# Kernel optimization log

Hardware: AMD Instinct MI355X
Metric: run time of the kernel (lower is better)

## Reference

```python
import jax, jax.numpy as jnp
from jax import lax
import numpy as np

T, N, E = 8, 20000, 640000
D_IN, H, K = 2, 64, 3


def setup_inputs() -> dict:
    key = jax.random.key(0)
    ks = jax.random.split(key, 10)
    x = jax.random.normal(ks[0], (T, N, D_IN), dtype=jnp.float32)
    edge_idx = jax.random.randint(ks[1], (T, 2, E), 0, N, dtype=jnp.int64)
    edge_attr = jax.random.uniform(ks[2], (T, E), dtype=jnp.float32)
    Fin = D_IN + H
    s = 0.05
    Wr = jax.random.normal(ks[3], (K, Fin, H), dtype=jnp.float32) * s
    Wu = jax.random.normal(ks[4], (K, Fin, H), dtype=jnp.float32) * s
    Wc = jax.random.normal(ks[5], (K, Fin, H), dtype=jnp.float32) * s
    br = jnp.zeros((H,), dtype=jnp.float32)
    bu = jnp.zeros((H,), dtype=jnp.float32)
    bc = jnp.zeros((H,), dtype=jnp.float32)
    return {"x": x, "edge_idx": edge_idx, "edge_attr": edge_attr,
            "Wr": Wr, "br": br, "Wu": Wu, "bu": bu, "Wc": Wc, "bc": bc}


def reference(x, edge_idx, edge_attr, Wr, br, Wu, bu, Wc, bc):
    n = x.shape[1]
    k_hops = Wr.shape[0]

    def cheb(v, src, dst, wn, W, b):
        # Chebyshev recursion on scaled Laplacian (PyG ChebConv, lambda_max=2)
        def prop(t):
            return jax.ops.segment_sum(wn[:, None] * t[src], dst, num_segments=n)
        Tx0 = v
        out = Tx0 @ W[0]
        Tx1 = prop(Tx0)
        out = out + Tx1 @ W[1]
        for kk in range(2, k_hops):
            Tx2 = 2.0 * prop(Tx1) - Tx0
            out = out + Tx2 @ W[kk]
            Tx0, Tx1 = Tx1, Tx2
        return out + b

    def step(h, inp):
        x_t, ei, w_t = inp
        src, dst = ei[0], ei[1]
        # sym-normalized Laplacian, scaled by 2/lambda_max=1; self-loop weight is 0
        deg = jax.ops.segment_sum(w_t, src, num_segments=n)
        safe = jnp.where(deg > 0, deg, 1.0)
        dinv = jnp.where(deg > 0, lax.rsqrt(safe), 0.0)
        wn = -dinv[src] * w_t * dinv[dst]
        comb = jnp.concatenate([x_t, h], axis=1)
        r = jax.nn.sigmoid(cheb(comb, src, dst, wn, Wr, br))
        u = jax.nn.sigmoid(cheb(comb, src, dst, wn, Wu, bu))
        c = jnp.tanh(cheb(jnp.concatenate([x_t, r * h], axis=1), src, dst, wn, Wc, bc))
        h_new = u * h + (1.0 - u) * c
        return h_new, None

    h0 = jnp.zeros((n, br.shape[0]), dtype=x.dtype)
    h_final, _ = lax.scan(step, h0, (x, edge_idx, edge_attr))
    return h_final
```

## Files before the change

### kernel.cpp

```cpp
#include <hip/hip_runtime.h>

#define NN 20000
#define EE 640000
#define TT 8
#define HF 64
#define AS 232
#define ACS 104
#define BSS 194
#define PBLK 5000
#define TILE 2560
#define NBIN 250
#define BWID 80
#define ECAP 3072
#define LCAP 24

typedef _Float16 f16;
typedef unsigned int uint;
typedef unsigned char uchar;
typedef __attribute__((ext_vector_type(8))) _Float16 half8;
typedef __attribute__((ext_vector_type(4))) float floatx4;

__device__ __forceinline__ float lo16f(uint v) { return (float)__builtin_bit_cast(f16, (unsigned short)(v & 0xffff)); }
__device__ __forceinline__ float hi16f(uint v) { return (float)__builtin_bit_cast(f16, (unsigned short)(v >> 16)); }
__device__ __forceinline__ uint pk16(float a, float b) {
    unsigned short ua = __builtin_bit_cast(unsigned short, (f16)a);
    unsigned short ub = __builtin_bit_cast(unsigned short, (f16)b);
    return (uint)ua | ((uint)ub << 16);
}

__global__ __launch_bounds__(256) void k_prepW(
    const float* __restrict__ Wr, const float* __restrict__ Wu, const float* __restrict__ Wc,
    f16* __restrict__ Wp, f16* __restrict__ Wcp)
{
    int idx = blockIdx.x * 256 + threadIdx.x;
    if (idx < 8 * 7 * 64) {
        int lane = idx & 63;
        int kb = (idx >> 6) % 7;
        int nb = (idx >> 6) / 7;
        int col = nb * 16 + (lane & 15);
        int g = col >> 6, jj = col & 63;
        const float* W = (g == 0) ? Wr : Wu;
        half8 v;
        #pragma unroll
        for (int e = 0; e < 8; e++) {
            int k = kb * 32 + ((lane >> 4) << 3) + e;
            float val = 0.f;
            if (k < 192)      { int hop = k >> 6; int i = 2 + (k & 63); val = W[(hop * 66 + i) * 64 + jj]; }
            else if (k < 198) { int q = k - 192;  int hop = q >> 1;     val = W[(hop * 66 + (q & 1)) * 64 + jj]; }
            v[e] = (f16)val;
        }
        *(half8*)&Wp[(size_t)idx * 8] = v;
        return;
    }
    int idx2 = idx - 8 * 7 * 64;
    if (idx2 >= 12 * 3 * 64) return;
    int lane = idx2 & 63;
    int kb = (idx2 >> 6) % 3;
    int nbc = (idx2 >> 6) / 3;
    int col = nbc * 16 + (lane & 15);
    int mode = col >> 6, j = col & 63;
    half8 v;
    #pragma unroll
    for (int e = 0; e < 8; e++) {
        int k = kb * 32 + ((lane >> 4) << 3) + e;
        float val = 0.f;
        if (k < 66) {
            if (mode == 0)      val = Wc[(0 * 66 + k) * 64 + j] - Wc[(2 * 66 + k) * 64 + j];
            else if (mode == 1) val = Wc[(1 * 66 + k) * 64 + j];
            else                val = Wc[(2 * 66 + k) * 64 + j];
        }
        v[e] = (f16)val;
    }
    *(half8*)&Wcp[(size_t)idx2 * 8] = v;
}

__global__ __launch_bounds__(256) void k_pack(
    const float* __restrict__ x, uint* __restrict__ xf)
{
    int idx = blockIdx.x * 256 + threadIdx.x;
    if (idx < TT * NN) xf[idx] = pk16(x[2 * idx], x[2 * idx + 1]);
}

__global__ __launch_bounds__(256) void k_bin(
    const int* __restrict__ eidx, const float* __restrict__ eatt,
    int* __restrict__ binptr, uint2* __restrict__ ebuf,
    int* __restrict__ sbinptr, uint* __restrict__ sbuf)
{
    __shared__ uint2 buf[NBIN][LCAP];
    __shared__ uint  sbl[NBIN][LCAP];
    __shared__ int lcnt[NBIN], scnt[NBIN];
    __shared__ int scan[256];
    __shared__ int gb[NBIN];
    int tid = threadIdx.x;
    if (tid < NBIN) { lcnt[tid] = 0; scnt[tid] = 0; }
    __syncthreads();
    int tl = blockIdx.x / 250, tile = blockIdx.x % 250;
    const int*   src = eidx + (size_t)tl * 2 * EE + tile * TILE;
    const int*   dst = src + EE;
    const float* w   = eatt + (size_t)tl * EE + tile * TILE;
    int* bp = binptr + tl * NBIN;
    int* sp = sbinptr + tl * NBIN;
    size_t ebase = (size_t)tl * NBIN * ECAP;
    #pragma unroll
    for (int i = 0; i < TILE / 256; i++) {
        int e = i * 256 + tid;
        int s = __builtin_nontemporal_load(&src[e]);
        int d = __builtin_nontemporal_load(&dst[e]);
        float wv = __builtin_nontemporal_load(&w[e]);
        int bin = d / BWID;
        uint2 ent = make_uint2(((uint)d << 16) | (uint)s, __float_as_uint(wv));
        int p = atomicAdd(&lcnt[bin], 1);
        if (p < LCAP) buf[bin][p] = ent;
        else {
            int gp = atomicAdd(&bp[bin], 1);
            if (gp < ECAP) ebuf[ebase + (size_t)bin * ECAP + gp] = ent;
        }
        int sbin = s / BWID;
        uint sent = (pk16(wv, 0.f) << 16) | (uint)s;
        int sq = atomicAdd(&scnt[sbin], 1);
        if (sq < LCAP) sbl[sbin][sq] = sent;
        else {
            int gp = atomicAdd(&sp[sbin], 1);
            if (gp < ECAP) sbuf[ebase + (size_t)sbin * ECAP + gp] = sent;
        }
    }
    __syncthreads();
    {
        int c = (tid < NBIN) ? (lcnt[tid] < LCAP ? lcnt[tid] : LCAP) : 0;
        scan[tid] = c;
        __syncthreads();
        #pragma unroll
        for (int o = 1; o < 256; o <<= 1) {
            int v = (tid >= o) ? scan[tid - o] : 0;
            __syncthreads();
            scan[tid] += v;
            __syncthreads();
        }
        if (c > 0) gb[tid] = atomicAdd(&bp[tid], c);
        __syncthreads();
        int total = scan[255];
        for (int i = tid; i < total; i += 256) {
            int lo = 0, hi = 255;
            #pragma unroll
            for (int it = 0; it < 8; it++) { int mid = (lo + hi) >> 1; if (scan[mid] > i) hi = mid; else lo = mid + 1; }
            int p = i - (lo ? scan[lo - 1] : 0);
            int gp = gb[lo] + p;
            if (gp < ECAP) ebuf[ebase + (size_t)lo * ECAP + gp] = buf[lo][p];
        }
    }
    __syncthreads();
    {
        int c = (tid < NBIN) ? (scnt[tid] < LCAP ? scnt[tid] : LCAP) : 0;
        scan[tid] = c;
        __syncthreads();
        #pragma unroll
        for (int o = 1; o < 256; o <<= 1) {
            int v = (tid >= o) ? scan[tid - o] : 0;
            __syncthreads();
            scan[tid] += v;
            __syncthreads();
        }
        if (c > 0) gb[tid] = atomicAdd(&sp[tid], c);
        __syncthreads();
        int total = scan[255];
        for (int i = tid; i < total; i += 256) {
            int lo = 0, hi = 255;
            #pragma unroll
            for (int it = 0; it < 8; it++) { int mid = (lo + hi) >> 1; if (scan[mid] > i) hi = mid; else lo = mid + 1; }
            int p = i - (lo ? scan[lo - 1] : 0);
            int gp = gb[lo] + p;
            if (gp < ECAP) sbuf[ebase + (size_t)lo * ECAP + gp] = sbl[lo][p];
        }
    }
}

__global__ __launch_bounds__(256) void k_degred(
    const uint* __restrict__ sbuf, const int* __restrict__ sbinptr,
    float* __restrict__ dinv)
{
    __shared__ float dacc[BWID];
    int tl = blockIdx.x / NBIN, b = blockIdx.x % NBIN, tid = threadIdx.x;
    int nume = sbinptr[tl * NBIN + b]; if (nume > ECAP) nume = ECAP;
    if (tid < BWID) dacc[tid] = 0.f;
    __syncthreads();
    size_t base = (size_t)(tl * NBIN + b) * ECAP;
    for (int i = tid; i < nume; i += 256) {
        uint e = sbuf[base + i];
        atomicAdd(&dacc[(e & 0xffff) - b * BWID], hi16f(e));
    }
    __syncthreads();
    if (tid < BWID) {
        float d = dacc[tid];
        dinv[(size_t)tl * NN + b * BWID + tid] = d > 0.f ? 1.f / sqrtf(d) : 0.f;
    }
}

__global__ __launch_bounds__(256) void k_csr(
    const uint2* __restrict__ ebuf, const int* __restrict__ binptr,
    const float* __restrict__ dinv,
    uint* __restrict__ entries, int* __restrict__ row_ptr, int* __restrict__ cnt)
{
    __shared__ uint proc[ECAP];
    __shared__ uchar lnb[ECAP];
    __shared__ uint staged[ECAP];
    __shared__ int lcnt[BWID], loff[BWID];
    int tl = blockIdx.x / NBIN, b = blockIdx.x % NBIN, tid = threadIdx.x;
    int nume = binptr[tl * NBIN + b]; if (nume > ECAP) nume = ECAP;
    const float* dv = dinv + (size_t)tl * NN;
    size_t base = (size_t)(tl * NBIN + b) * ECAP;
    if (tid < BWID) lcnt[tid] = 0;
    __syncthreads();
    for (int i = tid; i < nume; i += 256) {
        uint2 ent = ebuf[base + i];
        int s = ent.x & 0xffff;
        int d = ent.x >> 16;
        float wv = __uint_as_float(ent.y);
        float wn = -dv[s] * wv * dv[d];
        unsigned short wb = __builtin_bit_cast(unsigned short, (f16)wn);
        proc[i] = ((uint)wb << 16) | (uint)s;
        int ln = d - b * BWID;
        lnb[i] = (uchar)ln;
        atomicAdd(&lcnt[ln], 1);
    }
    __syncthreads();
    if (tid == 0) {
        int run = 0;
        for (int i = 0; i < BWID; i++) { loff[i] = run; run += lcnt[i]; }
    }
    __syncthreads();
    if (tid < BWID) {
        int n = tl * NN + b * BWID + tid;
        row_ptr[n] = (int)base + loff[tid];
        cnt[n] = lcnt[tid];
    }
    __syncthreads();
    for (int i = tid; i < nume; i += 256) {
        int p = atomicAdd(&loff[lnb[i]], 1);
        staged[p] = proc[i];
    }
    __syncthreads();
    for (int i = tid; i < nume; i += 256)
        entries[base + i] = staged[i];
}

__device__ __forceinline__ void gather64(
    const f16* __restrict__ src_mat, const uint* wnb, int mp, int j, int q,
    float& s0, float& s1)
{
    float a0[8], a1[8];
    #pragma unroll
    for (int k = 0; k < 8; k++) { a0[k] = 0.f; a1[k] = 0.f; }
    int e = 0;
    for (; e + 16 <= mp; e += 16) {
        uint ee[8], rr[8];
        #pragma unroll
        for (int k = 0; k < 8; k++) ee[k] = wnb[e + 2 * k + q];
        #pragma unroll
        for (int k = 0; k < 8; k++) rr[k] = *(const uint*)&src_mat[(size_t)(ee[k] & 0xffff) * HF + 2 * j];
        #pragma unroll
        for (int k = 0; k < 8; k++) {
            float w = hi16f(ee[k]);
            a0[k] += w * lo16f(rr[k]);
            a1[k] += w * hi16f(rr[k]);
        }
    }
    for (; e < mp; e += 8) {
        uint ee[4], rr[4];
        #pragma unroll
        for (int k = 0; k < 4; k++) ee[k] = wnb[e + 2 * k + q];
        #pragma unroll
        for (int k = 0; k < 4; k++) rr[k] = *(const uint*)&src_mat[(size_t)(ee[k] & 0xffff) * HF + 2 * j];
        #pragma unroll
        for (int k = 0; k < 4; k++) {
            float w = hi16f(ee[k]);
            a0[k] += w * lo16f(rr[k]);
            a1[k] += w * hi16f(rr[k]);
        }
    }
    s0 = ((a0[0] + a0[1]) + (a0[2] + a0[3])) + ((a0[4] + a0[5]) + (a0[6] + a0[7]));
    s1 = ((a1[0] + a1[1]) + (a1[2] + a1[3])) + ((a1[4] + a1[5]) + (a1[6] + a1[7]));
    s0 += __shfl_xor(s0, 32);
    s1 += __shfl_xor(s1, 32);
}

__global__ __launch_bounds__(256) void k_prop(
    const f16* __restrict__ src_mat, const f16* __restrict__ base,
    f16* __restrict__ dst,
    const int* __restrict__ row_ptr, const int* __restrict__ cnt,
    const uint* __restrict__ entries,
    float alpha, float beta,
    const uint* __restrict__ xsrc, const uint* __restrict__ xbase,
    uint* __restrict__ xdst)
{
    __shared__ uint wnbuf[4][128];
    int ws = threadIdx.x >> 6, lane = threadIdx.x & 63;
    int node = blockIdx.x * 4 + ws;
    int m = cnt[node]; if (m > 128) m = 128;
    int st = row_ptr[node];
    int mp = (m + 7) & ~7;
    for (int idx = lane; idx < mp; idx += 64)
        wnbuf[ws][idx] = (idx < m) ? entries[st + idx] : 0u;
    asm volatile("s_waitcnt lgkmcnt(0)" ::: "memory");

    int j = lane & 31, q = lane >> 5;
    float s0, s1;
    gather64(src_mat, wnbuf[ws], mp, j, q, s0, s1);
    if (q == 0) {
        float r0 = alpha * s0, r1 = alpha * s1;
        if (base) {
            uint bv = *(const uint*)&base[(size_t)node * HF + 2 * j];
            r0 += beta * lo16f(bv);
            r1 += beta * hi16f(bv);
        }
        *(uint*)&dst[(size_t)node * HF + 2 * j] = pk16(r0, r1);
    }

    if (xdst) {
        float xa0 = 0.f, xa1 = 0.f;
        for (int i = lane; i < mp; i += 64) {
            uint ent = wnbuf[ws][i];
            uint xv = xsrc[ent & 0xffff];
            float wn = hi16f(ent);
            xa0 += wn * lo16f(xv);
            xa1 += wn * hi16f(xv);
        }
        #pragma unroll
        for (int o = 32; o >= 1; o >>= 1) {
            xa0 += __shfl_xor(xa0, o);
            xa1 += __shfl_xor(xa1, o);
        }
        if (lane == 0) {
            float r0 = alpha * xa0, r1 = alpha * xa1;
            if (xbase) { uint bv = xbase[node]; r0 += beta * lo16f(bv); r1 += beta * hi16f(bv); }
            xdst[node] = pk16(r0, r1);
        }
    }
}

__global__ __launch_bounds__(256) void k_prop_fin(
    const f16* __restrict__ S, const f16* __restrict__ B0,
    const f16* __restrict__ u, const float* __restrict__ h_in,
    float* __restrict__ h_out, f16* __restrict__ hA_out,
    const int* __restrict__ row_ptr, const int* __restrict__ cnt,
    const uint* __restrict__ entries)
{
    __shared__ uint wnbuf[4][128];
    int ws = threadIdx.x >> 6, lane = threadIdx.x & 63;
    int node = blockIdx.x * 4 + ws;
    int m = cnt[node]; if (m > 128) m = 128;
    int st = row_ptr[node];
    int mp = (m + 7) & ~7;
    for (int idx = lane; idx < mp; idx += 64)
        wnbuf[ws][idx] = (idx < m) ? entries[st + idx] : 0u;
    asm volatile("s_waitcnt lgkmcnt(0)" ::: "memory");

    int j = lane & 31, q = lane >> 5;
    float s0, s1;
    gather64(S, wnbuf[ws], mp, j, q, s0, s1);
    if (q == 0) {
        uint b0v = *(const uint*)&B0[(size_t)node * HF + 2 * j];
        float c0 = tanhf(s0 + lo16f(b0v));
        float c1 = tanhf(s1 + hi16f(b0v));
        uint uv = *(const uint*)&u[(size_t)node * HF + 2 * j];
        float u0 = lo16f(uv), u1 = hi16f(uv);
        float2 hv = *(const float2*)&h_in[(size_t)node * HF + 2 * j];
        float hn0 = u0 * hv.x + (1.f - u0) * c0;
        float hn1 = u1 * hv.y + (1.f - u1) * c1;
        *(float2*)&h_out[(size_t)node * HF + 2 * j] = make_float2(hn0, hn1);
        *(uint*)&hA_out[(size_t)node * HF + 2 * j] = pk16(hn0, hn1);
    }
}

#define MFMA16(a, b, c) __builtin_amdgcn_mfma_f32_16x16x32_f16(a, b, c, 0, 0, 0)

__global__ __launch_bounds__(512) void k_ru(
    const f16* __restrict__ hA, const f16* __restrict__ t1, const f16* __restrict__ t2,
    const uint* __restrict__ xf, const uint* __restrict__ t1x, const uint* __restrict__ t2x,
    const f16* __restrict__ Wp, const f16* __restrict__ Wcp,
    const float* __restrict__ br, const float* __restrict__ bu, const float* __restrict__ bc,
    f16* __restrict__ u_out,
    f16* __restrict__ B0, f16* __restrict__ B1, f16* __restrict__ B2)
{
    __shared__ __attribute__((aligned(16))) f16 At[64][AS];
    __shared__ __attribute__((aligned(16))) f16 Ac[64][ACS];
    __shared__ f16 Ub[64][68];
    int n0 = blockIdx.x * 64;
    int tid = threadIdx.x;

    for (int idx = tid; idx < 64 * 8 * 3; idx += 512) {
        int a = idx >> 9, r = (idx >> 3) & 63, s = idx & 7;
        const f16* src = (a == 0) ? hA : (a == 1 ? t1 : t2);
        int gn = n0 + r;
        half8 v = {0, 0, 0, 0, 0, 0, 0, 0};
        if (gn < NN) v = *(const half8*)&src[(size_t)gn * HF + s * 8];
        *(half8*)&At[r][a * 64 + s * 8] = v;
    }
    for (int idx = tid; idx < 64 * 17; idx += 512) {
        int r = idx / 17, c = idx % 17;
        *(uint*)((char*)&At[r][198] + 4 * c) = 0u;
    }
    for (int idx = tid; idx < 64 * 3; idx += 512) {
        int r = idx & 63, a = idx >> 6;
        const uint* src = (a == 0) ? xf : (a == 1 ? t1x : t2x);
        int gn = n0 + r;
        uint v = 0;
        if (gn < NN) v = src[gn];
        *(uint*)&At[r][192 + 2 * a] = v;
    }
    for (int idx = tid; idx < 64; idx += 512) {
        int gn = n0 + idx;
        *(uint*)&Ac[idx][0] = (gn < NN) ? xf[gn] : 0u;
    }
    for (int idx = tid; idx < 64 * 15; idx += 512) {
        int r = idx / 15, c = idx % 15;
        *(uint*)((char*)&Ac[r][66] + 4 * c) = 0u;
    }
    __syncthreads();

    int wid = tid >> 6, lane = tid & 63;
    int mrow = (wid & 1) * 32;
    int nb0 = (wid >> 1) * 2;
    int arow = mrow + (lane & 15);
    int koff = (lane >> 4) << 3;
    floatx4 z = {0.f, 0.f, 0.f, 0.f};
    {
        floatx4 acc00 = z, acc01 = z, acc10 = z, acc11 = z;
        #pragma unroll
        for (int kb = 0; kb < 7; kb++) {
            half8 a0 = *(const half8*)&At[arow][kb * 32 + koff];
            half8 a1 = *(const half8*)&At[arow + 16][kb * 32 + koff];
            half8 b0 = *(const half8*)&Wp[(size_t)(((nb0    ) * 7 + kb) * 64 + lane) * 8];
            half8 b1 = *(const half8*)&Wp[(size_t)(((nb0 + 1) * 7 + kb) * 64 + lane) * 8];
            acc00 = MFMA16(a0, b0, acc00);
            acc10 = MFMA16(a1, b0, acc10);
            acc01 = MFMA16(a0, b1, acc01);
            acc11 = MFMA16(a1, b1, acc11);
        }
        bool isR = nb0 < 4;
        #pragma unroll
        for (int mi = 0; mi < 2; mi++) {
            #pragma unroll
            for (int ni = 0; ni < 2; ni++) {
                floatx4 a = (mi == 0) ? (ni == 0 ? acc00 : acc01) : (ni == 0 ? acc10 : acc11);
                int jj = ((nb0 + ni) * 16 + (lane & 15)) & 63;
                float bias = isR ? br[jj] : bu[jj];
                int rbase = mrow + mi * 16 + ((lane >> 4) << 2);
                #pragma unroll
                for (int e = 0; e < 4; e++) {
                    int rloc = rbase + e;
                    float s = 1.f / (1.f + __expf(-(a[e] + bias)));
                    if (isR) {
                        float hv = (float)At[rloc][jj];
                        Ac[rloc][2 + jj] = (f16)(s * hv);
                    } else {
                        Ub[rloc][jj] = (f16)s;
                    }
                }
            }
        }
    }
    __syncthreads();

    for (int idx = tid; idx < 64 * 32; idx += 512) {
        int n = idx >> 5, c = idx & 31;
        int gn = n0 + n;
        if (gn < NN) *(uint*)&u_out[(size_t)gn * HF + 2 * c] = *(uint*)&Ub[n][2 * c];
    }
    f16* Bs = &At[0][0];
    #pragma unroll
    for (int i = 0; i < 6; i++) {
        int t = wid * 6 + i;
        int nbc = t >> 2, mq = t & 3;
        int ar = mq * 16 + (lane & 15);
        floatx4 acc;
        float binit = (nbc < 4) ? bc[nbc * 16 + (lane & 15)] : 0.f;
        acc[0] = binit; acc[1] = binit; acc[2] = binit; acc[3] = binit;
        #pragma unroll
        for (int kb = 0; kb < 3; kb++) {
            half8 a = *(const half8*)&Ac[ar][kb * 32 + koff];
            half8 b = *(const half8*)&Wcp[(size_t)(((nbc * 3 + kb) * 64) + lane) * 8];
            acc = MFMA16(a, b, acc);
        }
        int rbase = mq * 16 + ((lane >> 4) << 2);
        int col = nbc * 16 + (lane & 15);
        #pragma unroll
        for (int e = 0; e < 4; e++)
            Bs[(size_t)(rbase + e) * BSS + col] = (f16)acc[e];
    }
    __syncthreads();

    for (int idx = tid; idx < 64 * 96; idx += 512) {
        int n = idx / 96, c = idx % 96;
        int gn = n0 + n;
        if (gn < NN) {
            int col = 2 * c;
            f16* Bdst = (col < 64) ? B0 : (col < 128 ? B1 : B2);
            *(uint*)&Bdst[(size_t)gn * HF + (col & 63)] = *(uint*)&Bs[(size_t)n * BSS + col];
        }
    }
}


extern "C" void kernel_launch(void* const* d_in, const int* in_sizes, int n_in,
                              void* d_out, int out_size, void* d_ws, size_t ws_size,
                              hipStream_t stream)
{
    const float* x    = (const float*)d_in[0];
    const int*   eidx = (const int*)d_in[1];
    const float* eatt = (const float*)d_in[2];
    const float* Wr   = (const float*)d_in[3];
    const float* br   = (const float*)d_in[4];
    const float* Wu   = (const float*)d_in[5];
    const float* bu   = (const float*)d_in[6];
    const float* Wc   = (const float*)d_in[7];
    const float* bc   = (const float*)d_in[8];

    char* ws = (char*)d_ws;
    size_t off = 0;
    auto alloc = [&](size_t bytes) -> void* {
        void* p = ws + off;
        off += (bytes + 255) & ~(size_t)255;
        return p;
    };
    const size_t FB = (size_t)NN * HF * 2;
    float* h_f32   = (float*)alloc((size_t)NN * HF * 4);
    f16*   hA      = (f16*)alloc(FB);
    f16*   t1      = (f16*)alloc(FB);
    f16*   t2      = (f16*)alloc(FB);
    f16*   u       = (f16*)alloc(FB);
    f16*   B0      = (f16*)alloc(FB);
    f16*   B1      = (f16*)alloc(FB);
    f16*   B2      = (f16*)alloc(FB);
    float* dinv    = (float*)alloc((size_t)TT * NN * 4);
    uint*  xf      = (uint*)alloc((size_t)TT * NN * 4);
    uint*  t1x     = (uint*)alloc((size_t)NN * 4);
    uint*  t2x     = (uint*)alloc((size_t)NN * 4);
    int*   bptr2   = (int*)alloc((size_t)2 * TT * NBIN * 4);
    uint2* ebuf    = (uint2*)alloc((size_t)TT * NBIN * ECAP * 8);
    uint*  sbuf    = (uint*)alloc((size_t)TT * NBIN * ECAP * 4);
    uint*  entr    = (uint*)alloc((size_t)TT * NBIN * ECAP * 4);
    int*   rowp    = (int*)alloc((size_t)TT * NN * 4);
    int*   cnt     = (int*)alloc((size_t)TT * NN * 4);
    f16*   Wp      = (f16*)alloc((size_t)8 * 7 * 64 * 8 * 2);
    f16*   Wcp     = (f16*)alloc((size_t)12 * 3 * 64 * 8 * 2);
    int* binptr = bptr2;
    int* sbinptr = bptr2 + TT * NBIN;

    hipMemsetAsync(h_f32, 0, (size_t)NN * HF * 4 + FB, stream);
    hipMemsetAsync(bptr2, 0, (size_t)2 * TT * NBIN * 4, stream);
    k_prepW<<<30, 256, 0, stream>>>(Wr, Wu, Wc, Wp, Wcp);
    k_pack <<<(TT * NN + 255) / 256, 256, 0, stream>>>(x, xf);

    k_bin   <<<TT * 250, 256, 0, stream>>>(eidx, eatt, binptr, ebuf, sbinptr, sbuf);
    k_degred<<<TT * NBIN, 256, 0, stream>>>(sbuf, sbinptr, dinv);
    k_csr   <<<TT * NBIN, 256, 0, stream>>>(ebuf, binptr, dinv, entr, rowp, cnt);

    const int GB = (NN + 63) / 64;

    for (int t = 0; t < TT; ++t) {
        const int* rp = rowp + (size_t)t * NN;
        const int* cp = cnt + (size_t)t * NN;
        uint* xft = xf + (size_t)t * NN;

        k_prop<<<PBLK, 256, 0, stream>>>(hA, nullptr, t1, rp, cp, entr, 1.f,  0.f, xft, nullptr, t1x);
        k_prop<<<PBLK, 256, 0, stream>>>(t1, hA,      t2, rp, cp, entr, 2.f, -1.f, t1x, xft,     t2x);

        k_ru<<<GB, 512, 0, stream>>>(hA, t1, t2, xft, t1x, t2x, Wp, Wcp,
                                     br, bu, bc, u, B0, B1, B2);

        k_prop<<<PBLK, 256, 0, stream>>>(B2, B1, t2, rp, cp, entr, 2.f, 1.f, nullptr, nullptr, nullptr);

        float* hdst = (t == TT - 1) ? (float*)d_out : h_f32;
        k_prop_fin<<<PBLK, 256, 0, stream>>>(t2, B0, u, h_f32, hdst, hA, rp, cp, entr);
    }
}
```

Before: 699.8 us.

## Fuse per-step kernels into one persistent kernel with software grid barriers

Replaces the degree, CSR and per-timestep propagation, gate and final kernels with a single persistent kernel of 512 blocks. Phases are separated by a flag-based global barrier that uses atomics and sleeps, and shared memory is reused across phases through a union. The aim is to remove about 40 kernel launch and drain gaps. The cost is lower parallelism per phase (512 blocks looping over work), gate blocks shrinking from 512 to 256 threads, and a deadlock risk if not all 512 blocks are co-resident.

```diff
diff --git a/kernel.cpp b/kernel.cpp
--- a/kernel.cpp
+++ b/kernel.cpp
@@ -13,6 +13,8 @@
 #define BWID 80
 #define ECAP 3072
 #define LCAP 24
+#define GRID 512
+#define GB 313
 
 typedef _Float16 f16;
 typedef unsigned int uint;
@@ -27,6 +29,8 @@
     unsigned short ub = __builtin_bit_cast(unsigned short, (f16)b);
     return (uint)ua | ((uint)ub << 16);
 }
+
+#define MFMA16(a, b, c) __builtin_amdgcn_mfma_f32_16x16x32_f16(a, b, c, 0, 0, 0)
 
 __global__ __launch_bounds__(256) void k_prepW(
     const float* __restrict__ Wr, const float* __restrict__ Wu, const float* __restrict__ Wc,
@@ -174,73 +178,51 @@
     }
 }
 
-__global__ __launch_bounds__(256) void k_degred(
-    const uint* __restrict__ sbuf, const int* __restrict__ sbinptr,
-    float* __restrict__ dinv)
-{
-    __shared__ float dacc[BWID];
-    int tl = blockIdx.x / NBIN, b = blockIdx.x % NBIN, tid = threadIdx.x;
-    int nume = sbinptr[tl * NBIN + b]; if (nume > ECAP) nume = ECAP;
-    if (tid < BWID) dacc[tid] = 0.f;
+union __attribute__((aligned(16))) SMem {
+    struct { f16 At[64][AS]; f16 Ac[64][ACS]; f16 Ub[64][68]; } g;
+    struct { uint proc[ECAP]; uint staged[ECAP]; uchar lnb[ECAP];
+             int lcnt[BWID]; int loff[BWID]; } c;
+    struct { float dacc[BWID]; } d;
+    uint wnbuf[4][128];
+};
+
+struct SP {
+    const uint2* ebuf; const uint* sbuf; const int* binptr; const int* sbinptr;
+    float* dinv; uint* entr; int* rowp; int* cnt;
+    const uint* xf; const f16* Wp; const f16* Wcp;
+    const float* br; const float* bu; const float* bc;
+    float* h; f16* hA; f16* t1; f16* t2; uint* t1x; uint* t2x;
+    f16* u; f16* B0; f16* B1; f16* B2; float* dout;
+    int* flags; int* gen;
+};
+
+__device__ __forceinline__ void gbar(int ph, int* flags, int* gen)
+{
     __syncthreads();
-    size_t base = (size_t)(tl * NBIN + b) * ECAP;
-    for (int i = tid; i < nume; i += 256) {
-        uint e = sbuf[base + i];
-        atomicAdd(&dacc[(e & 0xffff) - b * BWID], hi16f(e));
+    if (threadIdx.x == 0) {
+        __threadfence();
+        __hip_atomic_store(&flags[blockIdx.x], ph, __ATOMIC_RELEASE, __HIP_MEMORY_SCOPE_AGENT);
+    }
+    if (blockIdx.x == 0) {
+        if (threadIdx.x < 64) {
+            for (int b = threadIdx.x; b < GRID; b += 64)
+                while (__hip_atomic_load(&flags[b], __ATOMIC_RELAXED, __HIP_MEMORY_SCOPE_AGENT) < ph)
+                    __builtin_amdgcn_s_sleep(8);
+        }
+        __syncthreads();
+        if (threadIdx.x == 0) {
+            __threadfence();
+            __hip_atomic_store(gen, ph, __ATOMIC_RELEASE, __HIP_MEMORY_SCOPE_AGENT);
+        }
+    } else {
+        if (threadIdx.x == 0) {
+            while (__hip_atomic_load(gen, __ATOMIC_RELAXED, __HIP_MEMORY_SCOPE_AGENT) < ph)
+                __builtin_amdgcn_s_sleep(8);
+            __threadfence();
+        }
+        __syncthreads();
     }
     __syncthreads();
-    if (tid < BWID) {
-        float d = dacc[tid];
-        dinv[(size_t)tl * NN + b * BWID + tid] = d > 0.f ? 1.f / sqrtf(d) : 0.f;
-    }
-}
-
-__global__ __launch_bounds__(256) void k_csr(
-    const uint2* __restrict__ ebuf, const int* __restrict__ binptr,
-    const float* __restrict__ dinv,
-    uint* __restrict__ entries, int* __restrict__ row_ptr, int* __restrict__ cnt)
-{
-    __shared__ uint proc[ECAP];
-    __shared__ uchar lnb[ECAP];
-    __shared__ uint staged[ECAP];
-    __shared__ int lcnt[BWID], loff[BWID];
-    int tl = blockIdx.x / NBIN, b = blockIdx.x % NBIN, tid = threadIdx.x;
-    int nume = binptr[tl * NBIN + b]; if (nume > ECAP) nume = ECAP;
-    const float* dv = dinv + (size_t)tl * NN;
-    size_t base = (size_t)(tl * NBIN + b) * ECAP;
-    if (tid < BWID) lcnt[tid] = 0;
-    __syncthreads();
-    for (int i = tid; i < nume; i += 256) {
-        uint2 ent = ebuf[base + i];
-        int s = ent.x & 0xffff;
-        int d = ent.x >> 16;
-        float wv = __uint_as_float(ent.y);
-        float wn = -dv[s] * wv * dv[d];
-        unsigned short wb = __builtin_bit_cast(unsigned short, (f16)wn);
-        proc[i] = ((uint)wb << 16) | (uint)s;
-        int ln = d - b * BWID;
-        lnb[i] = (uchar)ln;
-        atomicAdd(&lcnt[ln], 1);
-    }
-    __syncthreads();
-    if (tid == 0) {
-        int run = 0;
-        for (int i = 0; i < BWID; i++) { loff[i] = run; run += lcnt[i]; }
-    }
-    __syncthreads();
-    if (tid < BWID) {
-        int n = tl * NN + b * BWID + tid;
-        row_ptr[n] = (int)base + loff[tid];
-        cnt[n] = lcnt[tid];
-    }
-    __syncthreads();
-    for (int i = tid; i < nume; i += 256) {
-        int p = atomicAdd(&loff[lnb[i]], 1);
-        staged[p] = proc[i];
-    }
-    __syncthreads();
-    for (int i = tid; i < nume; i += 256)
-        entries[base + i] = staged[i];
 }
 
 __device__ __forceinline__ void gather64(
@@ -283,220 +265,291 @@
     s1 += __shfl_xor(s1, 32);
 }
 
-__global__ __launch_bounds__(256) void k_prop(
-    const f16* __restrict__ src_mat, const f16* __restrict__ base,
-    f16* __restrict__ dst,
-    const int* __restrict__ row_ptr, const int* __restrict__ cnt,
-    const uint* __restrict__ entries,
+__device__ void prop_phase(
+    const f16* __restrict__ src_mat, const f16* __restrict__ base, f16* __restrict__ dst,
+    const int* __restrict__ rowp, const int* __restrict__ cntp, const uint* __restrict__ entries,
     float alpha, float beta,
-    const uint* __restrict__ xsrc, const uint* __restrict__ xbase,
-    uint* __restrict__ xdst)
-{
-    __shared__ uint wnbuf[4][128];
+    const uint* __restrict__ xsrc, const uint* __restrict__ xbase, uint* __restrict__ xdst,
+    uint (*wnbuf)[128])
+{
     int ws = threadIdx.x >> 6, lane = threadIdx.x & 63;
-    int node = blockIdx.x * 4 + ws;
-    int m = cnt[node]; if (m > 128) m = 128;
-    int st = row_ptr[node];
-    int mp = (m + 7) & ~7;
-    for (int idx = lane; idx < mp; idx += 64)
-        wnbuf[ws][idx] = (idx < m) ? entries[st + idx] : 0u;
-    asm volatile("s_waitcnt lgkmcnt(0)" ::: "memory");
-
-    int j = lane & 31, q = lane >> 5;
-    float s0, s1;
-    gather64(src_mat, wnbuf[ws], mp, j, q, s0, s1);
-    if (q == 0) {
-        float r0 = alpha * s0, r1 = alpha * s1;
-        if (base) {
-            uint bv = *(const uint*)&base[(size_t)node * HF + 2 * j];
-            r0 += beta * lo16f(bv);
-            r1 += beta * hi16f(bv);
-        }
-        *(uint*)&dst[(size_t)node * HF + 2 * j] = pk16(r0, r1);
-    }
-
-    if (xdst) {
-        float xa0 = 0.f, xa1 = 0.f;
-        for (int i = lane; i < mp; i += 64) {
-            uint ent = wnbuf[ws][i];
-            uint xv = xsrc[ent & 0xffff];
-            float wn = hi16f(ent);
-            xa0 += wn * lo16f(xv);
-            xa1 += wn * hi16f(xv);
-        }
-        #pragma unroll
-        for (int o = 32; o >= 1; o >>= 1) {
-            xa0 += __shfl_xor(xa0, o);
-            xa1 += __shfl_xor(xa1, o);
-        }
-        if (lane == 0) {
-            float r0 = alpha * xa0, r1 = alpha * xa1;
-            if (xbase) { uint bv = xbase[node]; r0 += beta * lo16f(bv); r1 += beta * hi16f(bv); }
-            xdst[node] = pk16(r0, r1);
-        }
-    }
-}
-
-__global__ __launch_bounds__(256) void k_prop_fin(
-    const f16* __restrict__ S, const f16* __restrict__ B0,
-    const f16* __restrict__ u, const float* __restrict__ h_in,
-    float* __restrict__ h_out, f16* __restrict__ hA_out,
-    const int* __restrict__ row_ptr, const int* __restrict__ cnt,
-    const uint* __restrict__ entries)
-{
-    __shared__ uint wnbuf[4][128];
+    for (int vb = blockIdx.x; vb < PBLK; vb += GRID) {
+        int node = vb * 4 + ws;
+        int m = cntp[node]; if (m > 128) m = 128;
+        int st = rowp[node];
+        int mp = (m + 7) & ~7;
+        for (int idx = lane; idx < mp; idx += 64)
+            wnbuf[ws][idx] = (idx < m) ? entries[st + idx] : 0u;
+        asm volatile("s_waitcnt lgkmcnt(0)" ::: "memory");
+        int j = lane & 31, q = lane >> 5;
+        float s0, s1;
+        gather64(src_mat, wnbuf[ws], mp, j, q, s0, s1);
+        if (q == 0) {
+            float r0 = alpha * s0, r1 = alpha * s1;
+            if (base) {
+                uint bv = *(const uint*)&base[(size_t)node * HF + 2 * j];
+                r0 += beta * lo16f(bv);
+                r1 += beta * hi16f(bv);
+            }
+            *(uint*)&dst[(size_t)node * HF + 2 * j] = pk16(r0, r1);
+        }
+        if (xdst) {
+            float xa0 = 0.f, xa1 = 0.f;
+            for (int i = lane; i < mp; i += 64) {
+                uint ent = wnbuf[ws][i];
+                uint xv = xsrc[ent & 0xffff];
+                float wn = hi16f(ent);
+                xa0 += wn * lo16f(xv);
+                xa1 += wn * hi16f(xv);
+            }
+            #pragma unroll
+            for (int o = 32; o >= 1; o >>= 1) {
+                xa0 += __shfl_xor(xa0, o);
+                xa1 += __shfl_xor(xa1, o);
+            }
+            if (lane == 0) {
+                float r0 = alpha * xa0, r1 = alpha * xa1;
+                if (xbase) { uint bv = xbase[node]; r0 += beta * lo16f(bv); r1 += beta * hi16f(bv); }
+                xdst[node] = pk16(r0, r1);
+            }
+        }
+    }
+}
+
+__device__ void fin_phase(const SP& p, const int* __restrict__ rowp, const int* __restrict__ cntp,
+                          float* __restrict__ h_out, uint (*wnbuf)[128])
+{
     int ws = threadIdx.x >> 6, lane = threadIdx.x & 63;
-    int node = blockIdx.x * 4 + ws;
-    int m = cnt[node]; if (m > 128) m = 128;
-    int st = row_ptr[node];
-    int mp = (m + 7) & ~7;
-    for (int idx = lane; idx < mp; idx += 64)
-        wnbuf[ws][idx] = (idx < m) ? entries[st + idx] : 0u;
-    asm volatile("s_waitcnt lgkmcnt(0)" ::: "memory");
-
-    int j = lane & 31, q = lane >> 5;
-    float s0, s1;
-    gather64(S, wnbuf[ws], mp, j, q, s0, s1);
-    if (q == 0) {
-        uint b0v = *(const uint*)&B0[(size_t)node * HF + 2 * j];
-        float c0 = tanhf(s0 + lo16f(b0v));
-        float c1 = tanhf(s1 + hi16f(b0v));
-        uint uv = *(const uint*)&u[(size_t)node * HF + 2 * j];
-        float u0 = lo16f(uv), u1 = hi16f(uv);
-        float2 hv = *(const float2*)&h_in[(size_t)node * HF + 2 * j];
-        float hn0 = u0 * hv.x + (1.f - u0) * c0;
-        float hn1 = u1 * hv.y + (1.f - u1) * c1;
-        *(float2*)&h_out[(size_t)node * HF + 2 * j] = make_float2(hn0, hn1);
-        *(uint*)&hA_out[(size_t)node * HF + 2 * j] = pk16(hn0, hn1);
-    }
-}
-
-#define MFMA16(a, b, c) __builtin_amdgcn_mfma_f32_16x16x32_f16(a, b, c, 0, 0, 0)
-
-__global__ __launch_bounds__(512) void k_ru(
-    const f16* __restrict__ hA, const f16* __restrict__ t1, const f16* __restrict__ t2,
-    const uint* __restrict__ xf, const uint* __restrict__ t1x, const uint* __restrict__ t2x,
-    const f16* __restrict__ Wp, const f16* __restrict__ Wcp,
-    const float* __restrict__ br, const float* __restrict__ bu, const float* __restrict__ bc,
-    f16* __restrict__ u_out,
-    f16* __restrict__ B0, f16* __restrict__ B1, f16* __restrict__ B2)
-{
-    __shared__ __attribute__((aligned(16))) f16 At[64][AS];
-    __shared__ __attribute__((aligned(16))) f16 Ac[64][ACS];
-    __shared__ f16 Ub[64][68];
-    int n0 = blockIdx.x * 64;
+    for (int vb = blockIdx.x; vb < PBLK; vb += GRID) {
+        int node = vb * 4 + ws;
+        int m = cntp[node]; if (m > 128) m = 128;
+        int st = rowp[node];
+        int mp = (m + 7) & ~7;
+        for (int idx = lane; idx < mp; idx += 64)
+            wnbuf[ws][idx] = (idx < m) ? p.entr[st + idx] : 0u;
+        asm volatile("s_waitcnt lgkmcnt(0)" ::: "memory");
+        int j = lane & 31, q = lane >> 5;
+        float s0, s1;
+        gather64(p.t2, wnbuf[ws], mp, j, q, s0, s1);
+        if (q == 0) {
+            uint b0v = *(const uint*)&p.B0[(size_t)node * HF + 2 * j];
+            float c0 = tanhf(s0 + lo16f(b0v));
+            float c1 = tanhf(s1 + hi16f(b0v));
+            uint uv = *(const uint*)&p.u[(size_t)node * HF + 2 * j];
+            float u0 = lo16f(uv), u1 = hi16f(uv);
+            float2 hv = *(const float2*)&p.h[(size_t)node * HF + 2 * j];
+            float hn0 = u0 * hv.x + (1.f - u0) * c0;
+            float hn1 = u1 * hv.y + (1.f - u1) * c1;
+            *(float2*)&h_out[(size_t)node * HF + 2 * j] = make_float2(hn0, hn1);
+            *(uint*)&p.hA[(size_t)node * HF + 2 * j] = pk16(hn0, hn1);
+        }
+    }
+}
+
+__device__ void gate_phase(const SP& p, SMem& sm, const uint* __restrict__ xft)
+{
     int tid = threadIdx.x;
-
-    for (int idx = tid; idx < 64 * 8 * 3; idx += 512) {
-        int a = idx >> 9, r = (idx >> 3) & 63, s = idx & 7;
-        const f16* src = (a == 0) ? hA : (a == 1 ? t1 : t2);
-        int gn = n0 + r;
-        half8 v = {0, 0, 0, 0, 0, 0, 0, 0};
-        if (gn < NN) v = *(const half8*)&src[(size_t)gn * HF + s * 8];
-        *(half8*)&At[r][a * 64 + s * 8] = v;
-    }
-    for (int idx = tid; idx < 64 * 17; idx += 512) {
-        int r = idx / 17, c = idx % 17;
-        *(uint*)((char*)&At[r][198] + 4 * c) = 0u;
-    }
-    for (int idx = tid; idx < 64 * 3; idx += 512) {
-        int r = idx & 63, a = idx >> 6;
-        const uint* src = (a == 0) ? xf : (a == 1 ? t1x : t2x);
-        int gn = n0 + r;
-        uint v = 0;
-        if (gn < NN) v = src[gn];
-        *(uint*)&At[r][192 + 2 * a] = v;
-    }
-    for (int idx = tid; idx < 64; idx += 512) {
-        int gn = n0 + idx;
-        *(uint*)&Ac[idx][0] = (gn < NN) ? xf[gn] : 0u;
-    }
-    for (int idx = tid; idx < 64 * 15; idx += 512) {
-        int r = idx / 15, c = idx % 15;
-        *(uint*)((char*)&Ac[r][66] + 4 * c) = 0u;
-    }
-    __syncthreads();
-
-    int wid = tid >> 6, lane = tid & 63;
-    int mrow = (wid & 1) * 32;
-    int nb0 = (wid >> 1) * 2;
-    int arow = mrow + (lane & 15);
-    int koff = (lane >> 4) << 3;
-    floatx4 z = {0.f, 0.f, 0.f, 0.f};
-    {
-        floatx4 acc00 = z, acc01 = z, acc10 = z, acc11 = z;
-        #pragma unroll
-        for (int kb = 0; kb < 7; kb++) {
-            half8 a0 = *(const half8*)&At[arow][kb * 32 + koff];
-            half8 a1 = *(const half8*)&At[arow + 16][kb * 32 + koff];
-            half8 b0 = *(const half8*)&Wp[(size_t)(((nb0    ) * 7 + kb) * 64 + lane) * 8];
-            half8 b1 = *(const half8*)&Wp[(size_t)(((nb0 + 1) * 7 + kb) * 64 + lane) * 8];
-            acc00 = MFMA16(a0, b0, acc00);
-            acc10 = MFMA16(a1, b0, acc10);
-            acc01 = MFMA16(a0, b1, acc01);
-            acc11 = MFMA16(a1, b1, acc11);
-        }
-        bool isR = nb0 < 4;
-        #pragma unroll
-        for (int mi = 0; mi < 2; mi++) {
+    for (int vb = blockIdx.x; vb < GB; vb += GRID) {
+        __syncthreads();
+        int n0 = vb * 64;
+        for (int idx = tid; idx < 64 * 8 * 3; idx += 256) {
+            int a = idx >> 9, r = (idx >> 3) & 63, s = idx & 7;
+            const f16* src = (a == 0) ? p.hA : (a == 1 ? p.t1 : p.t2);
+            int gn = n0 + r;
+            half8 v = {0, 0, 0, 0, 0, 0, 0, 0};
+            if (gn < NN) v = *(const half8*)&src[(size_t)gn * HF + s * 8];
+            *(half8*)&sm.g.At[r][a * 64 + s * 8] = v;
+        }
+        for (int idx = tid; idx < 64 * 17; idx += 256) {
+            int r = idx / 17, c = idx % 17;
+            *(uint*)((char*)&sm.g.At[r][198] + 4 * c) = 0u;
+        }
+        for (int idx = tid; idx < 64 * 3; idx += 256) {
+            int r = idx & 63, a = idx >> 6;
+            const uint* src = (a == 0) ? xft : (a == 1 ? p.t1x : p.t2x);
+            int gn = n0 + r;
+            uint v = 0;
+            if (gn < NN) v = src[gn];
+            *(uint*)&sm.g.At[r][192 + 2 * a] = v;
+        }
+        for (int idx = tid; idx < 64; idx += 256) {
+            int gn = n0 + idx;
+            *(uint*)&sm.g.Ac[idx][0] = (gn < NN) ? xft[gn] : 0u;
+        }
+        for (int idx = tid; idx < 64 * 15; idx += 256) {
+            int r = idx / 15, c = idx % 15;
+            *(uint*)((char*)&sm.g.Ac[r][66] + 4 * c) = 0u;
+        }
+        __syncthreads();
+
+        int wid = tid >> 6, lane = tid & 63;
+        int koff = (lane >> 4) << 3;
+        floatx4 z = {0.f, 0.f, 0.f, 0.f};
+        #pragma unroll
+        for (int sub = 0; sub < 2; sub++) {
+            int vw = (wid << 1) | sub;
+            int mrow = (vw & 1) * 32;
+            int nb0 = (vw >> 1) * 2;
+            int arow = mrow + (lane & 15);
+            floatx4 acc00 = z, acc01 = z, acc10 = z, acc11 = z;
             #pragma unroll
-            for (int ni = 0; ni < 2; ni++) {
-                floatx4 a = (mi == 0) ? (ni == 0 ? acc00 : acc01) : (ni == 0 ? acc10 : acc11);
-                int jj = ((nb0 + ni) * 16 + (lane & 15)) & 63;
-                float bias = isR ? br[jj] : bu[jj];
-                int rbase = mrow + mi * 16 + ((lane >> 4) << 2);
+            for (int kb = 0; kb < 7; kb++) {
+                half8 a0 = *(const half8*)&sm.g.At[arow][kb * 32 + koff];
+                half8 a1 = *(const half8*)&sm.g.At[arow + 16][kb * 32 + koff];
+                half8 b0 = *(const half8*)&p.Wp[(size_t)(((nb0    ) * 7 + kb) * 64 + lane) * 8];
+                half8 b1 = *(const half8*)&p.Wp[(size_t)(((nb0 + 1) * 7 + kb) * 64 + lane) * 8];
+                acc00 = MFMA16(a0, b0, acc00);
+                acc10 = MFMA16(a1, b0, acc10);
+                acc01 = MFMA16(a0, b1, acc01);
+                acc11 = MFMA16(a1, b1, acc11);
+            }
+            bool isR = nb0 < 4;
+            #pragma unroll
+            for (int mi = 0; mi < 2; mi++) {
                 #pragma unroll
-                for (int e = 0; e < 4; e++) {
-                    int rloc = rbase + e;
-                    float s = 1.f / (1.f + __expf(-(a[e] + bias)));
-                    if (isR) {
-                        float hv = (float)At[rloc][jj];
-                        Ac[rloc][2 + jj] = (f16)(s * hv);
-                    } else {
-                        Ub[rloc][jj] = (f16)s;
+                for (int ni = 0; ni < 2; ni++) {
+                    floatx4 a = (mi == 0) ? (ni == 0 ? acc00 : acc01) : (ni == 0 ? acc10 : acc11);
+                    int jj = ((nb0 + ni) * 16 + (lane & 15)) & 63;
+                    float bias = isR ? p.br[jj] : p.bu[jj];
+                    int rbase = mrow + mi * 16 + ((lane >> 4) << 2);
+                    #pragma unroll
+                    for (int e = 0; e < 4; e++) {
+                        int rloc = rbase + e;
+                        float s = 1.f / (1.f + __expf(-(a[e] + bias)));
+                        if (isR) {
+                            float hv = (float)sm.g.At[rloc][jj];
+                            sm.g.Ac[rloc][2 + jj] = (f16)(s * hv);
+                        } else {
+                            sm.g.Ub[rloc][jj] = (f16)s;
+                        }
                     }
                 }
             }
         }
-    }
-    __syncthreads();
-
-    for (int idx = tid; idx < 64 * 32; idx += 512) {
-        int n = idx >> 5, c = idx & 31;
-        int gn = n0 + n;
-        if (gn < NN) *(uint*)&u_out[(size_t)gn * HF + 2 * c] = *(uint*)&Ub[n][2 * c];
-    }
-    f16* Bs = &At[0][0];
-    #pragma unroll
-    for (int i = 0; i < 6; i++) {
-        int t = wid * 6 + i;
-        int nbc = t >> 2, mq = t & 3;
-        int ar = mq * 16 + (lane & 15);
-        floatx4 acc;
-        float binit = (nbc < 4) ? bc[nbc * 16 + (lane & 15)] : 0.f;
-        acc[0] = binit; acc[1] = binit; acc[2] = binit; acc[3] = binit;
-        #pragma unroll
-        for (int kb = 0; kb < 3; kb++) {
-            half8 a = *(const half8*)&Ac[ar][kb * 32 + koff];
-            half8 b = *(const half8*)&Wcp[(size_t)(((nbc * 3 + kb) * 64) + lane) * 8];
-            acc = MFMA16(a, b, acc);
-        }
-        int rbase = mq * 16 + ((lane >> 4) << 2);
-        int col = nbc * 16 + (lane & 15);
-        #pragma unroll
-        for (int e = 0; e < 4; e++)
-            Bs[(size_t)(rbase + e) * BSS + col] = (f16)acc[e];
-    }
-    __syncthreads();
-
-    for (int idx = tid; idx < 64 * 96; idx += 512) {
-        int n = idx / 96, c = idx % 96;
-        int gn = n0 + n;
-        if (gn < NN) {
-            int col = 2 * c;
-            f16* Bdst = (col < 64) ? B0 : (col < 128 ? B1 : B2);
-            *(uint*)&Bdst[(size_t)gn * HF + (col & 63)] = *(uint*)&Bs[(size_t)n * BSS + col];
-        }
+        __syncthreads();
+
+        for (int idx = tid; idx < 64 * 32; idx += 256) {
+            int n = idx >> 5, c = idx & 31;
+            int gn = n0 + n;
+            if (gn < NN) *(uint*)&p.u[(size_t)gn * HF + 2 * c] = *(uint*)&sm.g.Ub[n][2 * c];
+        }
+        f16* Bs = &sm.g.At[0][0];
+        #pragma unroll
+        for (int i = 0; i < 12; i++) {
+            int tt = wid * 12 + i;
+            int nbc = tt >> 2, mq = tt & 3;
+            int ar = mq * 16 + (lane & 15);
+            floatx4 acc;
+            float binit = (nbc < 4) ? p.bc[nbc * 16 + (lane & 15)] : 0.f;
+            acc[0] = binit; acc[1] = binit; acc[2] = binit; acc[3] = binit;
+            #pragma unroll
+            for (int kb = 0; kb < 3; kb++) {
+                half8 a = *(const half8*)&sm.g.Ac[ar][kb * 32 + koff];
+                half8 b = *(const half8*)&p.Wcp[(size_t)(((nbc * 3 + kb) * 64) + lane) * 8];
+                acc = MFMA16(a, b, acc);
+            }
+            int rbase = mq * 16 + ((lane >> 4) << 2);
+            int col = nbc * 16 + (lane & 15);
+            #pragma unroll
+            for (int e = 0; e < 4; e++)
+                Bs[(size_t)(rbase + e) * BSS + col] = (f16)acc[e];
+        }
+        __syncthreads();
+
+        for (int idx = tid; idx < 64 * 96; idx += 256) {
+            int n = idx / 96, c = idx % 96;
+            int gn = n0 + n;
+            if (gn < NN) {
+                int col = 2 * c;
+                f16* Bdst = (col < 64) ? p.B0 : (col < 128 ? p.B1 : p.B2);
+                *(uint*)&Bdst[(size_t)gn * HF + (col & 63)] = *(uint*)&Bs[(size_t)n * BSS + col];
+            }
+        }
+    }
+}
+
+__global__ __launch_bounds__(256, 2) void k_steps(SP p)
+{
+    __shared__ SMem sm;
+    int tid = threadIdx.x;
+    int ph = 0;
+
+    for (int vb = blockIdx.x; vb < TT * NBIN; vb += GRID) {
+        __syncthreads();
+        int tl = vb / NBIN, b = vb % NBIN;
+        int nume = p.sbinptr[tl * NBIN + b]; if (nume > ECAP) nume = ECAP;
+        if (tid < BWID) sm.d.dacc[tid] = 0.f;
+        __syncthreads();
+        size_t base = (size_t)(tl * NBIN + b) * ECAP;
+        for (int i = tid; i < nume; i += 256) {
+            uint e = p.sbuf[base + i];
+            atomicAdd(&sm.d.dacc[(e & 0xffff) - b * BWID], hi16f(e));
+        }
+        __syncthreads();
+        if (tid < BWID) {
+            float d = sm.d.dacc[tid];
+            p.dinv[(size_t)tl * NN + b * BWID + tid] = d > 0.f ? 1.f / sqrtf(d) : 0.f;
+        }
+    }
+    gbar(++ph, p.flags, p.gen);
+
+    for (int vb = blockIdx.x; vb < TT * NBIN; vb += GRID) {
+        __syncthreads();
+        int tl = vb / NBIN, b = vb % NBIN;
+        int nume = p.binptr[tl * NBIN + b]; if (nume > ECAP) nume = ECAP;
+        const float* dv = p.dinv + (size_t)tl * NN;
+        size_t base = (size_t)(tl * NBIN + b) * ECAP;
+        if (tid < BWID) sm.c.lcnt[tid] = 0;
+        __syncthreads();
+        for (int i = tid; i < nume; i += 256) {
+            uint2 ent = p.ebuf[base + i];
+            int s = ent.x & 0xffff;
+            int d = ent.x >> 16;
+            float wv = __uint_as_float(ent.y);
+            float wn = -dv[s] * wv * dv[d];
+            unsigned short wb = __builtin_bit_cast(unsigned short, (f16)wn);
+            sm.c.proc[i] = ((uint)wb << 16) | (uint)s;
+            int ln = d - b * BWID;
+            sm.c.lnb[i] = (uchar)ln;
+            atomicAdd(&sm.c.lcnt[ln], 1);
+        }
+        __syncthreads();
+        if (tid == 0) {
+            int run = 0;
+            for (int i = 0; i < BWID; i++) { sm.c.loff[i] = run; run += sm.c.lcnt[i]; }
+        }
+        __syncthreads();
+        if (tid < BWID) {
+            int n = tl * NN + b * BWID + tid;
+            p.rowp[n] = (int)base + sm.c.loff[tid];
+            p.cnt[n] = sm.c.lcnt[tid];
+        }
+        __syncthreads();
+        for (int i = tid; i < nume; i += 256) {
+            int pos = atomicAdd(&sm.c.loff[sm.c.lnb[i]], 1);
+            sm.c.staged[pos] = sm.c.proc[i];
+        }
+        __syncthreads();
+        for (int i = tid; i < nume; i += 256)
+            p.entr[base + i] = sm.c.staged[i];
+    }
+    gbar(++ph, p.flags, p.gen);
+
+    for (int t = 0; t < TT; t++) {
+        const int* rp = p.rowp + (size_t)t * NN;
+        const int* cp = p.cnt + (size_t)t * NN;
+        const uint* xft = p.xf + (size_t)t * NN;
+
+        prop_phase(p.hA, nullptr, p.t1, rp, cp, p.entr, 1.f, 0.f, xft, nullptr, p.t1x, sm.wnbuf);
+        gbar(++ph, p.flags, p.gen);
+        prop_phase(p.t1, p.hA, p.t2, rp, cp, p.entr, 2.f, -1.f, p.t1x, xft, p.t2x, sm.wnbuf);
+        gbar(++ph, p.flags, p.gen);
+        gate_phase(p, sm, xft);
+        gbar(++ph, p.flags, p.gen);
+        prop_phase(p.B2, p.B1, p.t2, rp, cp, p.entr, 2.f, 1.f, nullptr, nullptr, nullptr, sm.wnbuf);
+        gbar(++ph, p.flags, p.gen);
+        fin_phase(p, rp, cp, (t == TT - 1) ? p.dout : p.h, sm.wnbuf);
+        if (t < TT - 1) gbar(++ph, p.flags, p.gen);
     }
 }
 
@@ -543,34 +596,28 @@
     int*   cnt     = (int*)alloc((size_t)TT * NN * 4);
     f16*   Wp      = (f16*)alloc((size_t)8 * 7 * 64 * 8 * 2);
     f16*   Wcp     = (f16*)alloc((size_t)12 * 3 * 64 * 8 * 2);
+    int*   bar     = (int*)alloc(4096);
     int* binptr = bptr2;
     int* sbinptr = bptr2 + TT * NBIN;
+    int* flags = bar;
+    int* gen = bar + GRID;
 
     hipMemsetAsync(h_f32, 0, (size_t)NN * HF * 4 + FB, stream);
     hipMemsetAsync(bptr2, 0, (size_t)2 * TT * NBIN * 4, stream);
+    hipMemsetAsync(bar, 0, 4096, stream);
     k_prepW<<<30, 256, 0, stream>>>(Wr, Wu, Wc, Wp, Wcp);
     k_pack <<<(TT * NN + 255) / 256, 256, 0, stream>>>(x, xf);
 
-    k_bin   <<<TT * 250, 256, 0, stream>>>(eidx, eatt, binptr, ebuf, sbinptr, sbuf);
-    k_degred<<<TT * NBIN, 256, 0, stream>>>(sbuf, sbinptr, dinv);
-    k_csr   <<<TT * NBIN, 256, 0, stream>>>(ebuf, binptr, dinv, entr, rowp, cnt);
-
-    const int GB = (NN + 63) / 64;
-
-    for (int t = 0; t < TT; ++t) {
-        const int* rp = rowp + (size_t)t * NN;
-        const int* cp = cnt + (size_t)t * NN;
-        uint* xft = xf + (size_t)t * NN;
-
-        k_prop<<<PBLK, 256, 0, stream>>>(hA, nullptr, t1, rp, cp, entr, 1.f,  0.f, xft, nullptr, t1x);
-        k_prop<<<PBLK, 256, 0, stream>>>(t1, hA,      t2, rp, cp, entr, 2.f, -1.f, t1x, xft,     t2x);
-
-        k_ru<<<GB, 512, 0, stream>>>(hA, t1, t2, xft, t1x, t2x, Wp, Wcp,
-                                     br, bu, bc, u, B0, B1, B2);
-
-        k_prop<<<PBLK, 256, 0, stream>>>(B2, B1, t2, rp, cp, entr, 2.f, 1.f, nullptr, nullptr, nullptr);
-
-        float* hdst = (t == TT - 1) ? (float*)d_out : h_f32;
-        k_prop_fin<<<PBLK, 256, 0, stream>>>(t2, B0, u, h_f32, hdst, hA, rp, cp, entr);
-    }
-}
+    k_bin<<<TT * 250, 256, 0, stream>>>(eidx, eatt, binptr, ebuf, sbinptr, sbuf);
+
+    SP sp;
+    sp.ebuf = ebuf; sp.sbuf = sbuf; sp.binptr = binptr; sp.sbinptr = sbinptr;
+    sp.dinv = dinv; sp.entr = entr; sp.rowp = rowp; sp.cnt = cnt;
+    sp.xf = xf; sp.Wp = Wp; sp.Wcp = Wcp;
+    sp.br = br; sp.bu = bu; sp.bc = bc;
+    sp.h = h_f32; sp.hA = hA; sp.t1 = t1; sp.t2 = t2; sp.t1x = t1x; sp.t2x = t2x;
+    sp.u = u; sp.B0 = B0; sp.B1 = B1; sp.B2 = B2; sp.dout = (float*)d_out;
+    sp.flags = flags; sp.gen = gen;
+
+    k_steps<<<GRID, 256, 0, stream>>>(sp);
+}
```

Result: slower. 2.294 ms (+227.8%).

## Pad CSR rows to multiples of 8 and gather edge entries directly from global

Applied to the files above, without the earlier changes.

The CSR builder now pads each node's row to a multiple of 8 with zero entries, so the propagation kernels can read edge entries straight from global memory instead of first staging them into shared memory per wavefront. The binning kernel's flush of local buffers is simplified from a block-wide scan plus binary search to one thread per bin doing its own atomic reservation and copy. Bin capacity is raised and the local buffer depth lowered. This removes an LDS staging pass and the scan synchronisation, but relies on padded rows fitting in the larger bin capacity and makes the serial per-bin flush loop longer.

```diff
diff --git a/kernel.cpp b/kernel.cpp
--- a/kernel.cpp
+++ b/kernel.cpp
@@ -11,8 +11,8 @@
 #define TILE 2560
 #define NBIN 250
 #define BWID 80
-#define ECAP 3072
-#define LCAP 24
+#define ECAP 3840
+#define LCAP 16
 
 typedef _Float16 f16;
 typedef unsigned int uint;
@@ -27,6 +27,8 @@
     unsigned short ub = __builtin_bit_cast(unsigned short, (f16)b);
     return (uint)ua | ((uint)ub << 16);
 }
+
+#define MFMA16(a, b, c) __builtin_amdgcn_mfma_f32_16x16x32_f16(a, b, c, 0, 0, 0)
 
 __global__ __launch_bounds__(256) void k_prepW(
     const float* __restrict__ Wr, const float* __restrict__ Wu, const float* __restrict__ Wc,
@@ -89,8 +91,6 @@
     __shared__ uint2 buf[NBIN][LCAP];
     __shared__ uint  sbl[NBIN][LCAP];
     __shared__ int lcnt[NBIN], scnt[NBIN];
-    __shared__ int scan[256];
-    __shared__ int gb[NBIN];
     int tid = threadIdx.x;
     if (tid < NBIN) { lcnt[tid] = 0; scnt[tid] = 0; }
     __syncthreads();
@@ -125,51 +125,20 @@
         }
     }
     __syncthreads();
-    {
-        int c = (tid < NBIN) ? (lcnt[tid] < LCAP ? lcnt[tid] : LCAP) : 0;
-        scan[tid] = c;
-        __syncthreads();
-        #pragma unroll
-        for (int o = 1; o < 256; o <<= 1) {
-            int v = (tid >= o) ? scan[tid - o] : 0;
-            __syncthreads();
-            scan[tid] += v;
-            __syncthreads();
-        }
-        if (c > 0) gb[tid] = atomicAdd(&bp[tid], c);
-        __syncthreads();
-        int total = scan[255];
-        for (int i = tid; i < total; i += 256) {
-            int lo = 0, hi = 255;
-            #pragma unroll
-            for (int it = 0; it < 8; it++) { int mid = (lo + hi) >> 1; if (scan[mid] > i) hi = mid; else lo = mid + 1; }
-            int p = i - (lo ? scan[lo - 1] : 0);
-            int gp = gb[lo] + p;
-            if (gp < ECAP) ebuf[ebase + (size_t)lo * ECAP + gp] = buf[lo][p];
-        }
-    }
-    __syncthreads();
-    {
-        int c = (tid < NBIN) ? (scnt[tid] < LCAP ? scnt[tid] : LCAP) : 0;
-        scan[tid] = c;
-        __syncthreads();
-        #pragma unroll
-        for (int o = 1; o < 256; o <<= 1) {
-            int v = (tid >= o) ? scan[tid - o] : 0;
-            __syncthreads();
-            scan[tid] += v;
-            __syncthreads();
-        }
-        if (c > 0) gb[tid] = atomicAdd(&sp[tid], c);
-        __syncthreads();
-        int total = scan[255];
-        for (int i = tid; i < total; i += 256) {
-            int lo = 0, hi = 255;
-            #pragma unroll
-            for (int it = 0; it < 8; it++) { int mid = (lo + hi) >> 1; if (scan[mid] > i) hi = mid; else lo = mid + 1; }
-            int p = i - (lo ? scan[lo - 1] : 0);
-            int gp = gb[lo] + p;
-            if (gp < ECAP) sbuf[ebase + (size_t)lo * ECAP + gp] = sbl[lo][p];
+    if (tid < NBIN) {
+        int c = lcnt[tid]; if (c > LCAP) c = LCAP;
+        if (c > 0) {
+            int g = atomicAdd(&bp[tid], c);
+            uint2* dp = &ebuf[ebase + (size_t)tid * ECAP];
+            for (int i = 0; i < c; i++)
+                if (g + i < ECAP) dp[g + i] = buf[tid][i];
+        }
+        int cs = scnt[tid]; if (cs > LCAP) cs = LCAP;
+        if (cs > 0) {
+            int g = atomicAdd(&sp[tid], cs);
+            uint* dp = &sbuf[ebase + (size_t)tid * ECAP];
+            for (int i = 0; i < cs; i++)
+                if (g + i < ECAP) dp[g + i] = sbl[tid][i];
         }
     }
 }
@@ -204,6 +173,7 @@
     __shared__ uchar lnb[ECAP];
     __shared__ uint staged[ECAP];
     __shared__ int lcnt[BWID], loff[BWID];
+    __shared__ int ptot;
     int tl = blockIdx.x / NBIN, b = blockIdx.x % NBIN, tid = threadIdx.x;
     int nume = binptr[tl * NBIN + b]; if (nume > ECAP) nume = ECAP;
     const float* dv = dinv + (size_t)tl * NN;
@@ -225,9 +195,12 @@
     __syncthreads();
     if (tid == 0) {
         int run = 0;
-        for (int i = 0; i < BWID; i++) { loff[i] = run; run += lcnt[i]; }
-    }
-    __syncthreads();
+        for (int i = 0; i < BWID; i++) { loff[i] = run; run += (lcnt[i] + 7) & ~7; }
+        ptot = run <= ECAP ? run : ECAP;
+    }
+    __syncthreads();
+    int pt = ptot;
+    for (int i = tid; i < pt; i += 256) staged[i] = 0u;
     if (tid < BWID) {
         int n = tl * NN + b * BWID + tid;
         row_ptr[n] = (int)base + loff[tid];
@@ -236,15 +209,15 @@
     __syncthreads();
     for (int i = tid; i < nume; i += 256) {
         int p = atomicAdd(&loff[lnb[i]], 1);
-        staged[p] = proc[i];
-    }
-    __syncthreads();
-    for (int i = tid; i < nume; i += 256)
+        if (p < ECAP) staged[p] = proc[i];
+    }
+    __syncthreads();
+    for (int i = tid; i < pt; i += 256)
         entries[base + i] = staged[i];
 }
 
 __device__ __forceinline__ void gather64(
-    const f16* __restrict__ src_mat, const uint* wnb, int mp, int j, int q,
+    const f16* __restrict__ src_mat, const uint* __restrict__ wnb, int mp, int j, int q,
     float& s0, float& s1)
 {
     float a0[8], a1[8];
@@ -292,19 +265,15 @@
     const uint* __restrict__ xsrc, const uint* __restrict__ xbase,
     uint* __restrict__ xdst)
 {
-    __shared__ uint wnbuf[4][128];
     int ws = threadIdx.x >> 6, lane = threadIdx.x & 63;
     int node = blockIdx.x * 4 + ws;
     int m = cnt[node]; if (m > 128) m = 128;
-    int st = row_ptr[node];
     int mp = (m + 7) & ~7;
-    for (int idx = lane; idx < mp; idx += 64)
-        wnbuf[ws][idx] = (idx < m) ? entries[st + idx] : 0u;
-    asm volatile("s_waitcnt lgkmcnt(0)" ::: "memory");
+    const uint* wp = entries + row_ptr[node];
 
     int j = lane & 31, q = lane >> 5;
     float s0, s1;
-    gather64(src_mat, wnbuf[ws], mp, j, q, s0, s1);
+    gather64(src_mat, wp, mp, j, q, s0, s1);
     if (q == 0) {
         float r0 = alpha * s0, r1 = alpha * s1;
         if (base) {
@@ -318,7 +287,7 @@
     if (xdst) {
         float xa0 = 0.f, xa1 = 0.f;
         for (int i = lane; i < mp; i += 64) {
-            uint ent = wnbuf[ws][i];
+            uint ent = wp[i];
             uint xv = xsrc[ent & 0xffff];
             float wn = hi16f(ent);
             xa0 += wn * lo16f(xv);
@@ -344,19 +313,15 @@
     const int* __restrict__ row_ptr, const int* __restrict__ cnt,
     const uint* __restrict__ entries)
 {
-    __shared__ uint wnbuf[4][128];
     int ws = threadIdx.x >> 6, lane = threadIdx.x & 63;
     int node = blockIdx.x * 4 + ws;
     int m = cnt[node]; if (m > 128) m = 128;
-    int st = row_ptr[node];
     int mp = (m + 7) & ~7;
-    for (int idx = lane; idx < mp; idx += 64)
-        wnbuf[ws][idx] = (idx < m) ? entries[st + idx] : 0u;
-    asm volatile("s_waitcnt lgkmcnt(0)" ::: "memory");
+    const uint* wp = entries + row_ptr[node];
 
     int j = lane & 31, q = lane >> 5;
     float s0, s1;
-    gather64(S, wnbuf[ws], mp, j, q, s0, s1);
+    gather64(S, wp, mp, j, q, s0, s1);
     if (q == 0) {
         uint b0v = *(const uint*)&B0[(size_t)node * HF + 2 * j];
         float c0 = tanhf(s0 + lo16f(b0v));
@@ -370,8 +335,6 @@
         *(uint*)&hA_out[(size_t)node * HF + 2 * j] = pk16(hn0, hn1);
     }
 }
-
-#define MFMA16(a, b, c) __builtin_amdgcn_mfma_f32_16x16x32_f16(a, b, c, 0, 0, 0)
 
 __global__ __launch_bounds__(512) void k_ru(
     const f16* __restrict__ hA, const f16* __restrict__ t1, const f16* __restrict__ t2,
```

Measured after the change: 713.1 us. About the same (+1.9%).
